# Performance work log

Measured on AMD Instinct MI355X. Metric: run time of the kernel, lower is better.

The kernel has to match this reference:

```python
import jax, jax.numpy as jnp
import numpy as np

NEG = -1000.0  # matches the -1000 masking used in the original module


def setup_inputs() -> dict:
    key = jax.random.key(0)
    k0, k1, k2 = jax.random.split(key, 3)
    B, L, T = 512, 512, 32
    S = T + 2  # states: 0 = START, 1..T = tags, T+1 = STOP
    word_tag_value = jax.random.normal(k0, (B, L, T), dtype=jnp.float32)
    # xavier_uniform-style init for the transition matrix, then mask per the original
    a = float(np.sqrt(6.0 / (S + S)))
    translation = jax.random.uniform(k1, (S, S), dtype=jnp.float32, minval=-a, maxval=a)
    translation = translation.at[:, 0].set(NEG)       # nothing transitions into START
    translation = translation.at[S - 1, :].set(NEG)   # nothing transitions out of STOP
    real_tag = jax.random.randint(k2, (B, L), 1, T + 1)  # tags in 1..T
    return {"word_tag_value": word_tag_value, "translation": translation,
            "real_tag": real_tag, "output_loss": 1}


def _score_path(word_tag_value, translation, real_tag, T):
    # sum of emissions at the gold tags (tags 1..T index emission column tag-1)
    emit = jnp.take_along_axis(word_tag_value, (real_tag - 1)[..., None], axis=2)[..., 0]  # [B, L]
    score_emit = emit.sum(axis=1)
    # sum of transitions along the gold path + START/STOP transitions
    score_trans = translation[real_tag[:, :-1], real_tag[:, 1:]].sum(axis=1)
    score_trans = score_trans + translation[0, real_tag[:, 0]] + translation[real_tag[:, -1], T + 1]
    return score_emit + score_trans  # [B]


def _score_total(word_tag_value, translation, T):
    # forward algorithm (logsumexp recursion) over S = T+2 states
    B, L, _ = word_tag_value.shape
    # pad emissions to S states; START/STOP get NEG emission mid-sequence
    obs = jnp.pad(word_tag_value, ((0, 0), (0, 0), (1, 1)), constant_values=NEG)  # [B, L, S]
    # initial alpha: emissions of step 0 at tag states, 0 at START/STOP (as in original)
    alpha0 = jnp.pad(word_tag_value[:, 0, :], ((0, 0), (1, 1)), constant_values=0.0)  # [B, S]

    def step(alpha, obs_t):
        # scores[prev, cur] = alpha[prev] + obs_t[cur] + translation[prev, cur]
        m = alpha[:, :, None] + obs_t[:, None, :] + translation[None, :, :]  # [B, S, S]
        return jax.nn.logsumexp(m, axis=1), None

    alpha_T, _ = jax.lax.scan(step, alpha0, jnp.swapaxes(obs, 0, 1)[1:])  # scan over L-1 steps
    return jax.nn.logsumexp(alpha_T, axis=1)  # [B]


def reference(word_tag_value, translation, real_tag, output_loss):
    T = word_tag_value.shape[-1]
    if output_loss:
        return _score_total(word_tag_value, translation, T) - _score_path(word_tag_value, translation, real_tag, T)
    return None
```

## Files before the change

kernel.cpp:

```cpp
#include <hip/hip_runtime.h>


typedef float f32x2 __attribute__((ext_vector_type(2)));

#define F2   1.4426950408889634f
#define LN2  0.6931471805599453f
#define BIAS 0.0078125f
#define BIASCNT 3577

__device__ __forceinline__ float grpmax32(float x) {
    int t;
    t = __builtin_amdgcn_update_dpp(__float_as_int(x), __float_as_int(x), 0x121, 0xf, 0xf, true);
    x = fmaxf(x, __int_as_float(t));
    t = __builtin_amdgcn_update_dpp(__float_as_int(x), __float_as_int(x), 0x122, 0xf, 0xf, true);
    x = fmaxf(x, __int_as_float(t));
    t = __builtin_amdgcn_update_dpp(__float_as_int(x), __float_as_int(x), 0x124, 0xf, 0xf, true);
    x = fmaxf(x, __int_as_float(t));
    t = __builtin_amdgcn_update_dpp(__float_as_int(x), __float_as_int(x), 0x128, 0xf, 0xf, true);
    x = fmaxf(x, __int_as_float(t));
    t = __builtin_amdgcn_ds_swizzle(__float_as_int(x), 0x401F);
    x = fmaxf(x, __int_as_float(t));
    return x;
}

__global__ __launch_bounds__(64, 1) void crf_kernel(
    const float* __restrict__ wtv,
    const float* __restrict__ trans,
    const int*   __restrict__ rtag,
    float* __restrict__ out)
{
    __shared__ __align__(16) float tlds[1156];
    __shared__ __align__(16) int   ltag[1024];
    __shared__ __align__(16) float alds[160];

    const int l = threadIdx.x;
    const int q = l >> 5;
    const int c = l & 31;
    const int bbase = blockIdx.x * 2;

    for (int k = l; k < 1156; k += 64) tlds[k] = trans[k];
    {
        const int* rtb = rtag + (size_t)bbase * 512;
        for (int k = l; k < 1024; k += 64) ltag[k] = rtb[k];
    }
    __syncthreads();

    f32x2 tc2F[16], tc2B[16];
    #pragma unroll
    for (int k = 0; k < 16; ++k) {
        f32x2 vF, vB;
        vF.x = __builtin_exp2f(F2 * tlds[(2 * k + 1) * 34 + (c + 1)]) * BIAS;
        vF.y = __builtin_exp2f(F2 * tlds[(2 * k + 2) * 34 + (c + 1)]) * BIAS;
        vB.x = __builtin_exp2f(F2 * tlds[(c + 1) * 34 + (2 * k + 1)]) * BIAS;
        vB.y = __builtin_exp2f(F2 * tlds[(c + 1) * 34 + (2 * k + 2)]) * BIAS;
        tc2F[k] = vF;
        tc2B[k] = vB;
    }
    float aiF = __builtin_exp2f(F2 * tlds[c + 1]) * BIAS;

    const float* wbq = wtv + (size_t)(bbase + q) * (512 * 32);

    float stF = __builtin_exp2f(F2 * wbq[c]);
    float stB = 1.0f;
    int scF = 0, scB = 0;

    float vnF[16], vnB[16];
    #pragma unroll
    for (int j = 0; j < 8; ++j) {
        vnF[j] = wbq[(1 + j) * 32 + c];
        vnB[j] = wbq[(511 - j) * 32 + c];
    }
    float eoF_c = __builtin_exp2f(F2 * vnF[0]);
    float gB    = stB * __builtin_exp2f(F2 * vnB[0]);

    float* aF = alds + q * 36;
    float* aB = alds + 80 + q * 36;
    const float4* f4 = (const float4*)aF;
    const float4* b4 = (const float4*)aB;

    float4 ra[8], rb[8];

    aF[c] = stF;
    __builtin_amdgcn_wave_barrier();
    #pragma unroll
    for (int k = 0; k < 8; ++k) ra[k] = f4[k];
    __builtin_amdgcn_wave_barrier();

    for (int t0 = 1; t0 <= 241; t0 += 16) {
        #pragma unroll
        for (int j = 0; j < 16; ++j) {
            const int i = t0 + j;

            aB[c] = gB;
            __builtin_amdgcn_wave_barrier();
            #pragma unroll
            for (int k = 0; k < 8; ++k) rb[k] = b4[k];
            __builtin_amdgcn_wave_barrier();
            vnB[(j + 8) & 15] = wbq[(512 - (i + 8)) * 32 + c];
            float eoB_n = __builtin_exp2f(F2 * vnB[(j + 1) & 15]);
            {
                f32x2 a01 = {aiF, 0.0f};
                f32x2 a23 = {0.0f, 0.0f};
                aiF = 0.0f;
                #pragma unroll
                for (int k = 0; k < 8; ++k) {
                    float4 x = ra[k];
                    f32x2 xlo = {x.x, x.y};
                    f32x2 xhi = {x.z, x.w};
                    a01 = __builtin_elementwise_fma(xlo, tc2F[2 * k + 0], a01);
                    a23 = __builtin_elementwise_fma(xhi, tc2F[2 * k + 1], a23);
                }
                float s = (a01.x + a01.y) + (a23.x + a23.y);
                stF = s * eoF_c;
            }
            if (j == 15) {
                float m = grpmax32(stF);
                int e = ((__float_as_int(m) >> 23) & 0xff) - 127;
                stF *= __int_as_float((127 - e) << 23);
                scF += e;
            }

            aF[c] = stF;
            __builtin_amdgcn_wave_barrier();
            #pragma unroll
            for (int k = 0; k < 8; ++k) ra[k] = f4[k];
            __builtin_amdgcn_wave_barrier();
            vnF[(j + 8) & 15] = wbq[(i + 8) * 32 + c];
            float eoF_n = __builtin_exp2f(F2 * vnF[(j + 1) & 15]);
            {
                f32x2 a01 = {0.0f, 0.0f};
                f32x2 a23 = {0.0f, 0.0f};
                #pragma unroll
                for (int k = 0; k < 8; ++k) {
                    float4 x = rb[k];
                    f32x2 xlo = {x.x, x.y};
                    f32x2 xhi = {x.z, x.w};
                    a01 = __builtin_elementwise_fma(xlo, tc2B[2 * k + 0], a01);
                    a23 = __builtin_elementwise_fma(xhi, tc2B[2 * k + 1], a23);
                }
                float s = (a01.x + a01.y) + (a23.x + a23.y);
                if (j == 15) stB = (t0 != 241) ? s : stB;
                else         stB = s;
            }
            if (j == 15) {
                float m = grpmax32(stB);
                int e = ((__float_as_int(m) >> 23) & 0xff) - 127;
                stB *= __int_as_float((127 - e) << 23);
                scB += e;
            }
            gB    = stB * eoB_n;
            eoF_c = eoF_n;
        }
    }

    float prod = stF * stB;
    prod += __shfl_xor(prod, 1);
    prod += __shfl_xor(prod, 2);
    prod += __shfl_xor(prod, 4);
    prod += __shfl_xor(prod, 8);
    prod += __shfl_xor(prod, 16);
    float total = ((float)(scF + scB + BIASCNT) + __builtin_log2f(prod)) * LN2;

    float ps0 = 0.0f, ps1 = 0.0f;
    #pragma unroll
    for (int bb = 0; bb < 2; ++bb) {
        const float* w  = wtv + (size_t)(bbase + bb) * (512 * 32);
        const int*   tg = ltag + (bb << 9);
        int   tcur[8];
        float em[8];
        #pragma unroll
        for (int k = 0; k < 8; ++k) tcur[k] = tg[l + 64 * k];
        #pragma unroll
        for (int k = 0; k < 8; ++k) em[k] = w[(l + 64 * k) * 32 + (tcur[k] - 1)];
        float acc = 0.0f;
        #pragma unroll
        for (int k = 0; k < 8; ++k) {
            int t  = l + 64 * k;
            int nx = tg[(t + 1) & 511];
            nx = (t == 511) ? 33 : nx;
            acc += em[k] + tlds[tcur[k] * 34 + nx];
        }
        if (l == 0) acc += tlds[tg[0]];
        acc += __shfl_xor(acc, 1);
        acc += __shfl_xor(acc, 2);
        acc += __shfl_xor(acc, 4);
        acc += __shfl_xor(acc, 8);
        acc += __shfl_xor(acc, 16);
        acc += __shfl_xor(acc, 32);
        if (bb == 0) ps0 = acc; else ps1 = acc;
    }
    float ps = (q == 0) ? ps0 : ps1;
    if (c == 0) out[bbase + q] = total - ps;
}

extern "C" void kernel_launch(void* const* d_in, const int* in_sizes, int n_in,
                              void* d_out, int out_size, void* d_ws, size_t ws_size,
                              hipStream_t stream) {
    const float* wtv   = (const float*)d_in[0];
    const float* trans = (const float*)d_in[1];
    const int*   rtag  = (const int*)d_in[2];
    (void)in_sizes; (void)n_in; (void)d_ws; (void)ws_size; (void)out_size;
    float* out = (float*)d_out;
    crf_kernel<<<256, 64, 0, stream>>>(wtv, trans, rtag, out);
}
```

Before: 137.3 us.

## Split each batch's state reduction across both half-waves, one batch per block

Each block now handles a single batch element, and the two 32-lane halves of the wave each reduce over 16 of the 32 previous states. The halves are combined with a permlane32 swap. This halves the serial FMA chain and LDS reads per step of the forward/backward recursion, and doubles the grid from 256 to 512 blocks to use more CUs. In exchange it adds a cross-half exchange on the critical path of every step, and the wider grid may not fully fill or may oversubscribe the GPU.

```diff
diff --git a/kernel.cpp b/kernel.cpp
--- a/kernel.cpp
+++ b/kernel.cpp
@@ -21,6 +21,14 @@
     t = __builtin_amdgcn_ds_swizzle(__float_as_int(x), 0x401F);
     x = fmaxf(x, __int_as_float(t));
     return x;
+}
+
+__device__ __forceinline__ float xhalf_sum(float v) {
+    int a = __float_as_int(v);
+    int b;
+    asm("v_mov_b32 %0, %1" : "=v"(b) : "v"(a));
+    asm("v_permlane32_swap_b32 %0, %1" : "+v"(a), "+v"(b));
+    return __int_as_float(a) + __int_as_float(b);
 }
 
 __global__ __launch_bounds__(64, 1) void crf_kernel(
@@ -30,60 +38,66 @@
     float* __restrict__ out)
 {
     __shared__ __align__(16) float tlds[1156];
-    __shared__ __align__(16) int   ltag[1024];
-    __shared__ __align__(16) float alds[160];
+    __shared__ __align__(16) int   ltag[512];
+    __shared__ __align__(16) float alds[144];
 
     const int l = threadIdx.x;
-    const int q = l >> 5;
-    const int c = l & 31;
-    const int bbase = blockIdx.x * 2;
+    const int s = l & 31;
+    const int h = l >> 5;
+    const int b = blockIdx.x;
 
     for (int k = l; k < 1156; k += 64) tlds[k] = trans[k];
     {
-        const int* rtb = rtag + (size_t)bbase * 512;
-        for (int k = l; k < 1024; k += 64) ltag[k] = rtb[k];
+        const int* rtb = rtag + (size_t)b * 512;
+        for (int k = l; k < 512; k += 64) ltag[k] = rtb[k];
     }
     __syncthreads();
 
-    f32x2 tc2F[16], tc2B[16];
-    #pragma unroll
-    for (int k = 0; k < 16; ++k) {
-        f32x2 vF, vB;
-        vF.x = __builtin_exp2f(F2 * tlds[(2 * k + 1) * 34 + (c + 1)]) * BIAS;
-        vF.y = __builtin_exp2f(F2 * tlds[(2 * k + 2) * 34 + (c + 1)]) * BIAS;
-        vB.x = __builtin_exp2f(F2 * tlds[(c + 1) * 34 + (2 * k + 1)]) * BIAS;
-        vB.y = __builtin_exp2f(F2 * tlds[(c + 1) * 34 + (2 * k + 2)]) * BIAS;
-        tc2F[k] = vF;
-        tc2B[k] = vB;
-    }
-    float aiF = __builtin_exp2f(F2 * tlds[c + 1]) * BIAS;
-
-    const float* wbq = wtv + (size_t)(bbase + q) * (512 * 32);
-
-    float stF = __builtin_exp2f(F2 * wbq[c]);
+    f32x2 tcF2[8], tcB2[8];
+    #pragma unroll
+    for (int k = 0; k < 4; ++k) {
+        const int p0 = 16 * h + 4 * k;
+        f32x2 vA, vB, wA, wB2;
+        vA.x = __builtin_exp2f(F2 * tlds[(p0 + 1) * 34 + (s + 1)]) * BIAS;
+        vA.y = __builtin_exp2f(F2 * tlds[(p0 + 2) * 34 + (s + 1)]) * BIAS;
+        vB.x = __builtin_exp2f(F2 * tlds[(p0 + 3) * 34 + (s + 1)]) * BIAS;
+        vB.y = __builtin_exp2f(F2 * tlds[(p0 + 4) * 34 + (s + 1)]) * BIAS;
+        wA.x = __builtin_exp2f(F2 * tlds[(s + 1) * 34 + (p0 + 1)]) * BIAS;
+        wA.y = __builtin_exp2f(F2 * tlds[(s + 1) * 34 + (p0 + 2)]) * BIAS;
+        wB2.x = __builtin_exp2f(F2 * tlds[(s + 1) * 34 + (p0 + 3)]) * BIAS;
+        wB2.y = __builtin_exp2f(F2 * tlds[(s + 1) * 34 + (p0 + 4)]) * BIAS;
+        tcF2[2 * k] = vA; tcF2[2 * k + 1] = vB;
+        tcB2[2 * k] = wA; tcB2[2 * k + 1] = wB2;
+    }
+    float ai = (h == 0) ? __builtin_exp2f(F2 * tlds[s + 1]) * BIAS : 0.0f;
+
+    const float* wbq = wtv + (size_t)b * (512 * 32);
+    const float* wl  = wbq + s;
+
+    float stF = __builtin_exp2f(F2 * wl[0]);
     float stB = 1.0f;
     int scF = 0, scB = 0;
 
     float vnF[16], vnB[16];
     #pragma unroll
     for (int j = 0; j < 8; ++j) {
-        vnF[j] = wbq[(1 + j) * 32 + c];
-        vnB[j] = wbq[(511 - j) * 32 + c];
+        vnF[j] = wl[(1 + j) * 32];
+        vnB[j] = wl[(511 - j) * 32];
     }
     float eoF_c = __builtin_exp2f(F2 * vnF[0]);
-    float gB    = stB * __builtin_exp2f(F2 * vnB[0]);
-
-    float* aF = alds + q * 36;
-    float* aB = alds + 80 + q * 36;
-    const float4* f4 = (const float4*)aF;
-    const float4* b4 = (const float4*)aB;
-
-    float4 ra[8], rb[8];
-
-    aF[c] = stF;
+    float gB    = __builtin_exp2f(F2 * vnB[0]);
+
+    float* wF = alds;
+    float* wB = alds + 80;
+    const float4* rf4 = (const float4*)(alds + 16 * h);
+    const float4* rb4 = (const float4*)(alds + 80 + 16 * h);
+
+    float4 ra[4], rb[4];
+
+    wF[l] = stF;
     __builtin_amdgcn_wave_barrier();
     #pragma unroll
-    for (int k = 0; k < 8; ++k) ra[k] = f4[k];
+    for (int k = 0; k < 4; ++k) ra[k] = rf4[k];
     __builtin_amdgcn_wave_barrier();
 
     for (int t0 = 1; t0 <= 241; t0 += 16) {
@@ -91,27 +105,28 @@
         for (int j = 0; j < 16; ++j) {
             const int i = t0 + j;
 
-            aB[c] = gB;
+            wB[l] = gB;
             __builtin_amdgcn_wave_barrier();
             #pragma unroll
-            for (int k = 0; k < 8; ++k) rb[k] = b4[k];
-            __builtin_amdgcn_wave_barrier();
-            vnB[(j + 8) & 15] = wbq[(512 - (i + 8)) * 32 + c];
+            for (int k = 0; k < 4; ++k) rb[k] = rb4[k];
+            __builtin_amdgcn_wave_barrier();
+            vnB[(j + 8) & 15] = wl[(512 - (i + 8)) * 32];
             float eoB_n = __builtin_exp2f(F2 * vnB[(j + 1) & 15]);
             {
-                f32x2 a01 = {aiF, 0.0f};
+                f32x2 a01 = {ai, 0.0f};
                 f32x2 a23 = {0.0f, 0.0f};
-                aiF = 0.0f;
+                ai = 0.0f;
                 #pragma unroll
-                for (int k = 0; k < 8; ++k) {
+                for (int k = 0; k < 4; ++k) {
                     float4 x = ra[k];
                     f32x2 xlo = {x.x, x.y};
                     f32x2 xhi = {x.z, x.w};
-                    a01 = __builtin_elementwise_fma(xlo, tc2F[2 * k + 0], a01);
-                    a23 = __builtin_elementwise_fma(xhi, tc2F[2 * k + 1], a23);
+                    a01 = __builtin_elementwise_fma(xlo, tcF2[2 * k + 0], a01);
+                    a23 = __builtin_elementwise_fma(xhi, tcF2[2 * k + 1], a23);
                 }
-                float s = (a01.x + a01.y) + (a23.x + a23.y);
-                stF = s * eoF_c;
+                float part = (a01.x + a01.y) + (a23.x + a23.y);
+                float sum  = xhalf_sum(part);
+                stF = sum * eoF_c;
             }
             if (j == 15) {
                 float m = grpmax32(stF);
@@ -120,27 +135,27 @@
                 scF += e;
             }
 
-            aF[c] = stF;
+            wF[l] = stF;
             __builtin_amdgcn_wave_barrier();
             #pragma unroll
-            for (int k = 0; k < 8; ++k) ra[k] = f4[k];
-            __builtin_amdgcn_wave_barrier();
-            vnF[(j + 8) & 15] = wbq[(i + 8) * 32 + c];
+            for (int k = 0; k < 4; ++k) ra[k] = rf4[k];
+            __builtin_amdgcn_wave_barrier();
+            vnF[(j + 8) & 15] = wl[(i + 8) * 32];
             float eoF_n = __builtin_exp2f(F2 * vnF[(j + 1) & 15]);
             {
                 f32x2 a01 = {0.0f, 0.0f};
                 f32x2 a23 = {0.0f, 0.0f};
                 #pragma unroll
-                for (int k = 0; k < 8; ++k) {
+                for (int k = 0; k < 4; ++k) {
                     float4 x = rb[k];
                     f32x2 xlo = {x.x, x.y};
                     f32x2 xhi = {x.z, x.w};
-                    a01 = __builtin_elementwise_fma(xlo, tc2B[2 * k + 0], a01);
-                    a23 = __builtin_elementwise_fma(xhi, tc2B[2 * k + 1], a23);
+                    a01 = __builtin_elementwise_fma(xlo, tcB2[2 * k + 0], a01);
+                    a23 = __builtin_elementwise_fma(xhi, tcB2[2 * k + 1], a23);
                 }
-                float s = (a01.x + a01.y) + (a23.x + a23.y);
-                if (j == 15) stB = (t0 != 241) ? s : stB;
-                else         stB = s;
+                float part = (a01.x + a01.y) + (a23.x + a23.y);
+                float sum  = xhalf_sum(part);
+                stB = (i != 256) ? sum : stB;
             }
             if (j == 15) {
                 float m = grpmax32(stB);
@@ -161,36 +176,30 @@
     prod += __shfl_xor(prod, 16);
     float total = ((float)(scF + scB + BIASCNT) + __builtin_log2f(prod)) * LN2;
 
-    float ps0 = 0.0f, ps1 = 0.0f;
-    #pragma unroll
-    for (int bb = 0; bb < 2; ++bb) {
-        const float* w  = wtv + (size_t)(bbase + bb) * (512 * 32);
-        const int*   tg = ltag + (bb << 9);
-        int   tcur[8];
-        float em[8];
-        #pragma unroll
-        for (int k = 0; k < 8; ++k) tcur[k] = tg[l + 64 * k];
-        #pragma unroll
-        for (int k = 0; k < 8; ++k) em[k] = w[(l + 64 * k) * 32 + (tcur[k] - 1)];
-        float acc = 0.0f;
-        #pragma unroll
-        for (int k = 0; k < 8; ++k) {
-            int t  = l + 64 * k;
-            int nx = tg[(t + 1) & 511];
-            nx = (t == 511) ? 33 : nx;
-            acc += em[k] + tlds[tcur[k] * 34 + nx];
-        }
-        if (l == 0) acc += tlds[tg[0]];
-        acc += __shfl_xor(acc, 1);
-        acc += __shfl_xor(acc, 2);
-        acc += __shfl_xor(acc, 4);
-        acc += __shfl_xor(acc, 8);
-        acc += __shfl_xor(acc, 16);
-        acc += __shfl_xor(acc, 32);
-        if (bb == 0) ps0 = acc; else ps1 = acc;
-    }
-    float ps = (q == 0) ? ps0 : ps1;
-    if (c == 0) out[bbase + q] = total - ps;
+    const int* tg = ltag;
+    int   tcur[8];
+    float em[8];
+    #pragma unroll
+    for (int k = 0; k < 8; ++k) tcur[k] = tg[l + 64 * k];
+    #pragma unroll
+    for (int k = 0; k < 8; ++k) em[k] = wbq[(l + 64 * k) * 32 + (tcur[k] - 1)];
+    float acc = 0.0f;
+    #pragma unroll
+    for (int k = 0; k < 8; ++k) {
+        int t  = l + 64 * k;
+        int nx = tg[(t + 1) & 511];
+        nx = (t == 511) ? 33 : nx;
+        acc += em[k] + tlds[tcur[k] * 34 + nx];
+    }
+    if (l == 0) acc += tlds[tg[0]];
+    acc += __shfl_xor(acc, 1);
+    acc += __shfl_xor(acc, 2);
+    acc += __shfl_xor(acc, 4);
+    acc += __shfl_xor(acc, 8);
+    acc += __shfl_xor(acc, 16);
+    acc += __shfl_xor(acc, 32);
+
+    if (l == 0) out[b] = total - acc;
 }
 
 extern "C" void kernel_launch(void* const* d_in, const int* in_sizes, int n_in,
@@ -201,5 +210,5 @@
     const int*   rtag  = (const int*)d_in[2];
     (void)in_sizes; (void)n_in; (void)d_ws; (void)ws_size; (void)out_size;
     float* out = (float*)d_out;
-    crf_kernel<<<256, 64, 0, stream>>>(wtv, trans, rtag, out);
-}
+    crf_kernel<<<512, 64, 0, stream>>>(wtv, trans, rtag, out);
+}
```

After: 120.9 us. -12.0%, faster.
